# Kernel tuning notes

Hardware: AMD Instinct MI355X
Metric: run time of the kernel (lower is better)

The kernel has to match this reference:

```python
import jax, jax.numpy as jnp
import numpy as np

BLOCK_SIZE = 64
N_EMBD = 128
N_HEAD = 4
HEAD_DIM = N_EMBD // N_HEAD  # 32


def setup_inputs() -> dict:
    key = jax.random.key(0)
    kx, kq, kk, kv = jax.random.split(key, 4)
    B, T = 4096, 64
    x = jax.random.normal(kx, (B, T, N_EMBD), dtype=jnp.float32)
    # nn.Linear(n_embd, head_dim, bias=False): stored as [out,in] in torch,
    # here kept as [in, out] = [128, 32] so projection is x @ W.
    s = 1.0 / np.sqrt(N_EMBD)
    Wq = jax.random.uniform(kq, (N_EMBD, HEAD_DIM), jnp.float32, -s, s)
    Wk = jax.random.uniform(kk, (N_EMBD, HEAD_DIM), jnp.float32, -s, s)
    Wv = jax.random.uniform(kv, (N_EMBD, HEAD_DIM), jnp.float32, -s, s)
    return {"x": x, "Wq": Wq, "Wk": Wk, "Wv": Wv}


def reference(x, Wq, Wk, Wv):
    B, T, C = x.shape
    q = x @ Wq  # [B, T, Hd]
    k = x @ Wk
    v = x @ Wv
    scale = 1.0 / jnp.sqrt(jnp.asarray(k.shape[-1], x.dtype))
    wei = jnp.einsum("btd,bsd->bts", q, k) * scale  # [B, T, T]
    causal = jnp.tril(jnp.ones((T, T), dtype=bool))
    wei = jnp.where(causal, wei, -jnp.inf)
    wei = jax.nn.softmax(wei, axis=-1)
    out = jnp.einsum("bts,bsd->btd", wei, v)  # [B, T, Hd]
    return out
```

## Files before the change

### kernel.cpp

```cpp
#include <hip/hip_runtime.h>


#define TT 64
#define CC 128
#define HD 32

typedef __bf16 bf16_t;
typedef __bf16 bf8_t __attribute__((ext_vector_type(8)));
typedef __bf16 bf4_t __attribute__((ext_vector_type(4)));
typedef float  f4_t  __attribute__((ext_vector_type(4)));

__global__ __launch_bounds__(256) void prep_weights(
    const float* __restrict__ Wq, const float* __restrict__ Wk,
    const float* __restrict__ Wv, bf16_t* __restrict__ wf)
{
  int t = blockIdx.x * 256 + threadIdx.x;
  int j    = t & 7;
  int lane = (t >> 3) & 63;
  int kt   = (t >> 9) & 3;
  int n6   = t >> 11;
  int k    = kt * 32 + (lane >> 4) * 8 + j;
  int col  = (n6 & 1) * 16 + (lane & 15);
  const float* W = (n6 >> 1) == 0 ? Wq : ((n6 >> 1) == 1 ? Wk : Wv);
  float v = W[k * HD + col];
  if (n6 < 2) v *= 0.17677669529663687f;
  wf[t] = (bf16_t)v;
}

__global__ __launch_bounds__(64, 2) void head_fused(
    const float* __restrict__ x, const bf8_t* __restrict__ wf,
    float* __restrict__ out)
{
  __shared__ __align__(16) bf16_t qs[TT][40];
  __shared__ __align__(16) bf16_t ks[TT][40];
  __shared__ __align__(16) bf16_t vt[HD][72];
  __shared__ __align__(16) bf16_t ps[16][72];

  const int lane = threadIdx.x;
  const int quad = lane >> 4;
  const int l16  = lane & 15;
  const int b    = blockIdx.x;
  const float* __restrict__ xblk = x + (size_t)b * (TT * CC);
  float* __restrict__ ob = out + (size_t)b * (TT * HD);

  const f4_t zero4 = {0.f, 0.f, 0.f, 0.f};

  bf8_t wfr[24];
  float4 qf[2];

  auto load_q = [&](int i, int p) {
    const float* s = xblk + (16 * i + l16) * CC + p * 32 + quad * 8;
    qf[0] = *(const float4*)s;
    qf[1] = *(const float4*)(s + 4);
  };
  auto cvtq = [&]() -> bf8_t {
    float4 f0 = qf[0], f1 = qf[1];
    bf8_t a;
    a[0] = (bf16_t)f0.x; a[1] = (bf16_t)f0.y; a[2] = (bf16_t)f0.z; a[3] = (bf16_t)f0.w;
    a[4] = (bf16_t)f1.x; a[5] = (bf16_t)f1.y; a[6] = (bf16_t)f1.z; a[7] = (bf16_t)f1.w;
    return a;
  };

  auto proj_tile = [&](int i) {
    f4_t acc[6];
    #pragma unroll
    for (int n = 0; n < 6; ++n) acc[n] = zero4;
    #pragma unroll
    for (int p = 0; p < 4; ++p) {
      bf8_t a = cvtq();
      if (p < 3)      load_q(i, p + 1);
      else if (i < 3) load_q(i + 1, 0);
      #pragma unroll
      for (int n = 0; n < 6; ++n)
        acc[n] = __builtin_amdgcn_mfma_f32_16x16x32_bf16(a, wfr[n * 4 + p], acc[n], 0, 0, 0);
    }
    #pragma unroll
    for (int r = 0; r < 4; ++r) {
      int row = 16 * i + quad * 4 + r;
      qs[row][l16]      = (bf16_t)acc[0][r];
      qs[row][16 + l16] = (bf16_t)acc[1][r];
      ks[row][l16]      = (bf16_t)acc[2][r];
      ks[row][16 + l16] = (bf16_t)acc[3][r];
    }
    bf4_t v0 = { (bf16_t)acc[4][0], (bf16_t)acc[4][1], (bf16_t)acc[4][2], (bf16_t)acc[4][3] };
    bf4_t v1 = { (bf16_t)acc[5][0], (bf16_t)acc[5][1], (bf16_t)acc[5][2], (bf16_t)acc[5][3] };
    *(bf4_t*)&vt[l16][16 * i + quad * 4]      = v0;
    *(bf4_t*)&vt[16 + l16][16 * i + quad * 4] = v1;
  };

  bf8_t ones8;
  #pragma unroll
  for (int t = 0; t < 8; ++t) ones8[t] = (bf16_t)1.0f;

  auto sm_tile = [&](int i) {
    f4_t sc[4];
    bf8_t aq = *(const bf8_t*)&qs[16 * i + l16][quad * 8];
    #pragma unroll
    for (int j = 0; j < 4; ++j) {
      sc[j] = zero4;
      if (j <= i) {
        bf8_t bk = *(const bf8_t*)&ks[16 * j + l16][quad * 8];
        sc[j] = __builtin_amdgcn_mfma_f32_16x16x32_bf16(aq, bk, zero4, 0, 0, 0);
      }
    }
    #pragma unroll
    for (int r = 0; r < 4; ++r) {
      int rl = quad * 4 + r;
      #pragma unroll
      for (int j = 0; j < 4; ++j) {
        if (j <= i) {
          bool valid = (j < i) | (l16 <= rl);
          float e = __expf(sc[j][r]);
          ps[rl][j * 16 + l16] = (bf16_t)(valid ? e : 0.f);
        } else if (j == (i | 1)) {
          ps[rl][j * 16 + l16] = (bf16_t)0.f;
        }
      }
    }
    f4_t o0 = zero4, o1 = zero4, osum = zero4;
    #pragma unroll
    for (int kk = 0; kk <= (i >> 1); ++kk) {
      int k0 = kk * 32 + quad * 8;
      bf8_t ap  = *(const bf8_t*)&ps[l16][k0];
      bf8_t bv0 = *(const bf8_t*)&vt[l16][k0];
      bf8_t bv1 = *(const bf8_t*)&vt[16 + l16][k0];
      o0   = __builtin_amdgcn_mfma_f32_16x16x32_bf16(ap, bv0, o0, 0, 0, 0);
      o1   = __builtin_amdgcn_mfma_f32_16x16x32_bf16(ap, bv1, o1, 0, 0, 0);
      osum = __builtin_amdgcn_mfma_f32_16x16x32_bf16(ap, ones8, osum, 0, 0, 0);
    }
    #pragma unroll
    for (int r = 0; r < 4; ++r) {
      int row = 16 * i + quad * 4 + r;
      float inv = __builtin_amdgcn_rcpf(osum[r]);
      ob[row * HD + l16]      = o0[r] * inv;
      ob[row * HD + 16 + l16] = o1[r] * inv;
    }
  };

  load_q(0, 0);
  #pragma unroll
  for (int t = 0; t < 24; ++t) wfr[t] = wf[t * 64 + lane];
  proj_tile(0);
  proj_tile(1);
  proj_tile(2);
  proj_tile(3);
  sm_tile(0);
  sm_tile(1);
  sm_tile(2);
  sm_tile(3);
}

extern "C" void kernel_launch(void* const* d_in, const int* in_sizes, int n_in,
                              void* d_out, int out_size, void* d_ws, size_t ws_size,
                              hipStream_t stream) {
  const float* x  = (const float*)d_in[0];
  const float* Wq = (const float*)d_in[1];
  const float* Wk = (const float*)d_in[2];
  const float* Wv = (const float*)d_in[3];
  float* out = (float*)d_out;
  bf16_t* wf = (bf16_t*)d_ws;
  int B = in_sizes[0] / (TT * CC);

  prep_weights<<<dim3(48), dim3(256), 0, stream>>>(Wq, Wk, Wv, wf);
  head_fused<<<dim3(B), dim3(64), 0, stream>>>(x, (const bf8_t*)wf, out);
}
```

Measured before the change: 208.9 us.

## Split each batch block across four waves and stage weights in LDS

Each batch element now runs on a 256-thread block with four waves, one per 16-row tile, in place of a single wave processing all four tiles serially. The projection weights are staged once per block in shared memory rather than held in 24 registers per lane, and the score/probability buffer reuses the weight LDS region after a barrier. This raises parallelism and cuts register pressure, at the cost of block barriers, one weight copy into LDS per block, and wave load imbalance from the causal mask.

```diff
diff --git a/kernel.cpp b/kernel.cpp
--- a/kernel.cpp
+++ b/kernel.cpp
@@ -27,16 +27,17 @@
   wf[t] = (bf16_t)v;
 }
 
-__global__ __launch_bounds__(64, 2) void head_fused(
-    const float* __restrict__ x, const bf8_t* __restrict__ wf,
+__global__ __launch_bounds__(256) void head_fused(
+    const float* __restrict__ x, const float4* __restrict__ wf,
     float* __restrict__ out)
 {
-  __shared__ __align__(16) bf16_t qs[TT][40];
+  __shared__ __align__(16) bf16_t wlds[12288];
   __shared__ __align__(16) bf16_t ks[TT][40];
   __shared__ __align__(16) bf16_t vt[HD][72];
-  __shared__ __align__(16) bf16_t ps[16][72];
 
-  const int lane = threadIdx.x;
+  const int tid  = threadIdx.x;
+  const int wv   = tid >> 6;
+  const int lane = tid & 63;
   const int quad = lane >> 4;
   const int l16  = lane & 15;
   const int b    = blockIdx.x;
@@ -45,11 +46,10 @@
 
   const f4_t zero4 = {0.f, 0.f, 0.f, 0.f};
 
-  bf8_t wfr[24];
   float4 qf[2];
 
-  auto load_q = [&](int i, int p) {
-    const float* s = xblk + (16 * i + l16) * CC + p * 32 + quad * 8;
+  auto load_q = [&](int p) {
+    const float* s = xblk + (16 * wv + l16) * CC + p * 32 + quad * 8;
     qf[0] = *(const float4*)s;
     qf[1] = *(const float4*)(s + 4);
   };
@@ -61,93 +61,100 @@
     return a;
   };
 
-  auto proj_tile = [&](int i) {
-    f4_t acc[6];
+  load_q(0);
+  #pragma unroll
+  for (int u = 0; u < 6; ++u) {
+    float4 w4 = wf[u * 256 + tid];
+    *(float4*)&wlds[(size_t)(u * 256 + tid) * 8] = w4;
+  }
+  __syncthreads();
+
+  auto wfrag = [&](int t) -> bf8_t {
+    return *(const bf8_t*)&wlds[t * 512 + lane * 8];
+  };
+
+  f4_t acc[6];
+  #pragma unroll
+  for (int n = 0; n < 6; ++n) acc[n] = zero4;
+  #pragma unroll
+  for (int p = 0; p < 4; ++p) {
+    bf8_t a = cvtq();
+    if (p < 3) load_q(p + 1);
     #pragma unroll
-    for (int n = 0; n < 6; ++n) acc[n] = zero4;
-    #pragma unroll
-    for (int p = 0; p < 4; ++p) {
-      bf8_t a = cvtq();
-      if (p < 3)      load_q(i, p + 1);
-      else if (i < 3) load_q(i + 1, 0);
-      #pragma unroll
-      for (int n = 0; n < 6; ++n)
-        acc[n] = __builtin_amdgcn_mfma_f32_16x16x32_bf16(a, wfr[n * 4 + p], acc[n], 0, 0, 0);
-    }
-    #pragma unroll
-    for (int r = 0; r < 4; ++r) {
-      int row = 16 * i + quad * 4 + r;
-      qs[row][l16]      = (bf16_t)acc[0][r];
-      qs[row][16 + l16] = (bf16_t)acc[1][r];
-      ks[row][l16]      = (bf16_t)acc[2][r];
-      ks[row][16 + l16] = (bf16_t)acc[3][r];
-    }
-    bf4_t v0 = { (bf16_t)acc[4][0], (bf16_t)acc[4][1], (bf16_t)acc[4][2], (bf16_t)acc[4][3] };
-    bf4_t v1 = { (bf16_t)acc[5][0], (bf16_t)acc[5][1], (bf16_t)acc[5][2], (bf16_t)acc[5][3] };
-    *(bf4_t*)&vt[l16][16 * i + quad * 4]      = v0;
-    *(bf4_t*)&vt[16 + l16][16 * i + quad * 4] = v1;
-  };
+    for (int n = 0; n < 6; ++n)
+      acc[n] = __builtin_amdgcn_mfma_f32_16x16x32_bf16(a, wfrag(n * 4 + p), acc[n], 0, 0, 0);
+  }
+  #pragma unroll
+  for (int r = 0; r < 4; ++r) {
+    int row = 16 * wv + quad * 4 + r;
+    ks[row][l16]      = (bf16_t)acc[2][r];
+    ks[row][16 + l16] = (bf16_t)acc[3][r];
+  }
+  bf4_t v0 = { (bf16_t)acc[4][0], (bf16_t)acc[4][1], (bf16_t)acc[4][2], (bf16_t)acc[4][3] };
+  bf4_t v1 = { (bf16_t)acc[5][0], (bf16_t)acc[5][1], (bf16_t)acc[5][2], (bf16_t)acc[5][3] };
+  *(bf4_t*)&vt[l16][16 * wv + quad * 4]      = v0;
+  *(bf4_t*)&vt[16 + l16][16 * wv + quad * 4] = v1;
+  bf4_t qc0 = { (bf16_t)acc[0][0], (bf16_t)acc[0][1], (bf16_t)acc[0][2], (bf16_t)acc[0][3] };
+  bf4_t qc1 = { (bf16_t)acc[1][0], (bf16_t)acc[1][1], (bf16_t)acc[1][2], (bf16_t)acc[1][3] };
+  __syncthreads();
+
+  bf16_t* __restrict__ psw = wlds + wv * 1152;
+
+  #pragma unroll
+  for (int r = 0; r < 4; ++r) {
+    psw[(quad * 4 + r) * 72 + l16]      = qc0[r];
+    psw[(quad * 4 + r) * 72 + 16 + l16] = qc1[r];
+  }
+  bf8_t aq = *(const bf8_t*)&psw[l16 * 72 + quad * 8];
 
   bf8_t ones8;
   #pragma unroll
   for (int t = 0; t < 8; ++t) ones8[t] = (bf16_t)1.0f;
 
-  auto sm_tile = [&](int i) {
-    f4_t sc[4];
-    bf8_t aq = *(const bf8_t*)&qs[16 * i + l16][quad * 8];
+  const int i = wv;
+  f4_t sc[4];
+  #pragma unroll
+  for (int j = 0; j < 4; ++j) {
+    sc[j] = zero4;
+    if (j <= i) {
+      bf8_t bk = *(const bf8_t*)&ks[16 * j + l16][quad * 8];
+      sc[j] = __builtin_amdgcn_mfma_f32_16x16x32_bf16(aq, bk, zero4, 0, 0, 0);
+    }
+  }
+  #pragma unroll
+  for (int r = 0; r < 4; ++r) {
+    int rl = quad * 4 + r;
     #pragma unroll
     for (int j = 0; j < 4; ++j) {
-      sc[j] = zero4;
       if (j <= i) {
-        bf8_t bk = *(const bf8_t*)&ks[16 * j + l16][quad * 8];
-        sc[j] = __builtin_amdgcn_mfma_f32_16x16x32_bf16(aq, bk, zero4, 0, 0, 0);
+        bool valid = (j < i) | (l16 <= rl);
+        float e = __expf(sc[j][r]);
+        psw[rl * 72 + j * 16 + l16] = (bf16_t)(valid ? e : 0.f);
+      } else if (j == (i | 1)) {
+        psw[rl * 72 + j * 16 + l16] = (bf16_t)0.f;
       }
     }
-    #pragma unroll
-    for (int r = 0; r < 4; ++r) {
-      int rl = quad * 4 + r;
-      #pragma unroll
-      for (int j = 0; j < 4; ++j) {
-        if (j <= i) {
-          bool valid = (j < i) | (l16 <= rl);
-          float e = __expf(sc[j][r]);
-          ps[rl][j * 16 + l16] = (bf16_t)(valid ? e : 0.f);
-        } else if (j == (i | 1)) {
-          ps[rl][j * 16 + l16] = (bf16_t)0.f;
-        }
-      }
-    }
-    f4_t o0 = zero4, o1 = zero4, osum = zero4;
-    #pragma unroll
-    for (int kk = 0; kk <= (i >> 1); ++kk) {
+  }
+  f4_t o0 = zero4, o1 = zero4, osum = zero4;
+  #pragma unroll
+  for (int kk = 0; kk < 2; ++kk) {
+    if (kk <= (i >> 1)) {
       int k0 = kk * 32 + quad * 8;
-      bf8_t ap  = *(const bf8_t*)&ps[l16][k0];
+      bf8_t ap  = *(const bf8_t*)&psw[l16 * 72 + k0];
       bf8_t bv0 = *(const bf8_t*)&vt[l16][k0];
       bf8_t bv1 = *(const bf8_t*)&vt[16 + l16][k0];
       o0   = __builtin_amdgcn_mfma_f32_16x16x32_bf16(ap, bv0, o0, 0, 0, 0);
       o1   = __builtin_amdgcn_mfma_f32_16x16x32_bf16(ap, bv1, o1, 0, 0, 0);
       osum = __builtin_amdgcn_mfma_f32_16x16x32_bf16(ap, ones8, osum, 0, 0, 0);
     }
-    #pragma unroll
-    for (int r = 0; r < 4; ++r) {
-      int row = 16 * i + quad * 4 + r;
-      float inv = __builtin_amdgcn_rcpf(osum[r]);
-      ob[row * HD + l16]      = o0[r] * inv;
-      ob[row * HD + 16 + l16] = o1[r] * inv;
-    }
-  };
-
-  load_q(0, 0);
+  }
   #pragma unroll
-  for (int t = 0; t < 24; ++t) wfr[t] = wf[t * 64 + lane];
-  proj_tile(0);
-  proj_tile(1);
-  proj_tile(2);
-  proj_tile(3);
-  sm_tile(0);
-  sm_tile(1);
-  sm_tile(2);
-  sm_tile(3);
+  for (int r = 0; r < 4; ++r) {
+    int row = 16 * i + quad * 4 + r;
+    float inv = __builtin_amdgcn_rcpf(osum[r]);
+    ob[row * HD + l16]      = o0[r] * inv;
+    ob[row * HD + 16 + l16] = o1[r] * inv;
+  }
 }
 
 extern "C" void kernel_launch(void* const* d_in, const int* in_sizes, int n_in,
@@ -162,5 +169,5 @@
   int B = in_sizes[0] / (TT * CC);
 
   prep_weights<<<dim3(48), dim3(256), 0, stream>>>(Wq, Wk, Wv, wf);
-  head_fused<<<dim3(B), dim3(64), 0, stream>>>(x, (const bf8_t*)wf, out);
+  head_fused<<<dim3(B), dim3(256), 0, stream>>>(x, (const float4*)wf, out);
 }
```

After: 206.1 us. About the same (-1.3%).
